# Kernel tuning notes

Hardware: AMD Instinct MI355X
Metric: run time of the kernel (lower is better)

## Reference

```python
import jax, jax.numpy as jnp
import numpy as np

INSTANCES = 4
ALPHA = 0.99
N, D_IN, C = 4096, 512, 512


def setup_inputs() -> dict:
    key = jax.random.key(0)
    k1, k2 = jax.random.split(key)
    x = jax.random.normal(k1, (N, D_IN), dtype=jnp.float32)
    Wb = jax.random.normal(k2, (D_IN, C), dtype=jnp.float32) / np.sqrt(D_IN).astype(np.float32)
    gamma = jnp.ones((2,), dtype=jnp.float32)
    return {"x": x, "Wb": Wb, "gamma": gamma}


def reference(x, Wb, gamma):
    # base model: linear feature extractor -> [N, C]
    f = x @ Wb
    n, c = f.shape
    f = f.reshape(n // INSTANCES, INSTANCES, c)
    probe = f[:, 0, :].reshape(-1, c)                 # [P, C]
    gallery = f[:, 1:INSTANCES, :].reshape(-1, c)     # [G, C]

    def embed(a, b):
        # pairwise squared distance via GEMM (no [len(a),len(b),C] tensor)
        d2 = (jnp.sum(a * a, axis=1)[:, None]
              + jnp.sum(b * b, axis=1)[None, :]
              - 2.0 * (a @ b.T)) / c
        return jnp.stack([jnp.exp(-gamma[0] * d2), gamma[1] * d2], axis=-1)

    p_g = embed(probe, gallery)     # [P, G, 2]
    g_g = embed(gallery, gallery)   # [G, G, 2]
    G = g_g.shape[0]

    gg0 = g_g[:, :, 0]
    # D = diag(1 / off-diagonal row sums); A = D @ gg0
    off_rowsum = jnp.sum(gg0, axis=1) - jnp.diagonal(gg0)
    A = gg0 / off_rowsum[:, None]
    # closed-form random-walk fixed point: (1-alpha) * (I - alpha A)^-1, then transpose
    A = (1.0 - ALPHA) * jnp.linalg.inv(jnp.eye(G, dtype=gg0.dtype) - ALPHA * A)
    A = A.T

    pg0 = p_g[:, :, 0] @ A          # rescored probe-gallery scores
    p_g = p_g.at[:, :, 0].set(pg0)

    score = jnp.concatenate([p_g.reshape(-1, 2), g_g.reshape(-1, 2)], axis=0)
    return score
```

## Files before the change

### kernel.cpp

```cpp
#include <hip/hip_runtime.h>

typedef unsigned short u16;
typedef short short8v __attribute__((ext_vector_type(8)));
typedef float f32x4 __attribute__((ext_vector_type(4)));
typedef float f32x2 __attribute__((ext_vector_type(2)));
typedef unsigned short u16x4 __attribute__((ext_vector_type(4)));

#define ALPHA_C 0.99f
#define NITER 2
#define WS_NEEDED 67500000UL

__device__ __forceinline__ u16 f2bf(float f){
  union { float f; unsigned u; } v; v.f = f;
  unsigned r = (v.u + 0x7FFFu + ((v.u >> 16) & 1u)) >> 16;
  return (u16)r;
}
__device__ __forceinline__ float bf2f(u16 u){
  union { unsigned u; float f; } v; v.u = ((unsigned)u) << 16;
  return v.f;
}

__device__ __forceinline__ void gload16(const void* g, void* l){
  __builtin_amdgcn_global_load_lds(
    (const __attribute__((address_space(1))) unsigned*)g,
    (__attribute__((address_space(3))) unsigned*)l, 16, 0, 0);
}

__device__ __forceinline__ float blockSumBcast(float v){
  #pragma unroll
  for(int off=32; off>0; off>>=1) v += __shfl_down(v, off, 64);
  __shared__ float sm[4];
  __shared__ float res;
  int w = threadIdx.x >> 6;
  if((threadIdx.x & 63)==0) sm[w] = v;
  __syncthreads();
  if(threadIdx.x==0) res = sm[0]+sm[1]+sm[2]+sm[3];
  __syncthreads();
  return res;
}

__global__ void k_canary(float* out){ out[0] = 12345.0f; }

__global__ void k_wbt(const float* __restrict__ Wb, u16* __restrict__ Wbt){
  __shared__ float t[32][33];
  int bx = blockIdx.x & 15, by = blockIdx.x >> 4;
  int tx = threadIdx.x & 31, ty = threadIdx.x >> 5;
  #pragma unroll
  for(int i=0;i<32;i+=8)
    t[ty+i][tx] = Wb[(by*32+ty+i)*512 + bx*32+tx];
  __syncthreads();
  #pragma unroll
  for(int i=0;i<32;i+=8)
    Wbt[(bx*32+ty+i)*512 + by*32 + tx] = f2bf(t[tx][ty+i]);
}

__global__ void k_f2bf8(const float* __restrict__ in, u16* __restrict__ out, int n8){
  int i = blockIdx.x*256 + threadIdx.x;
  if(i >= n8) return;
  f32x4 a = *reinterpret_cast<const f32x4*>(in + (size_t)i*8);
  f32x4 b = *reinterpret_cast<const f32x4*>(in + (size_t)i*8 + 4);
  short8v o;
  o[0]=(short)f2bf(a[0]); o[1]=(short)f2bf(a[1]); o[2]=(short)f2bf(a[2]); o[3]=(short)f2bf(a[3]);
  o[4]=(short)f2bf(b[0]); o[5]=(short)f2bf(b[1]); o[6]=(short)f2bf(b[2]); o[7]=(short)f2bf(b[3]);
  *reinterpret_cast<short8v*>(out + (size_t)i*8) = o;
}

__global__ void __launch_bounds__(256) k_gemm(
    int epi,
    const u16* __restrict__ A, const u16* __restrict__ B,
    int kld, int nbn, int bps, int kspan,
    const float* __restrict__ nrmA, const float* __restrict__ nrmB,
    const float* __restrict__ gamma,
    u16* __restrict__ u0, u16* __restrict__ u1,
    float* __restrict__ fo0,
    float* __restrict__ f0, const float* __restrict__ f1)
{
  int bid = blockIdx.x;
  int slice, brow, bcol;
  if(epi==3){
    int L = (bid & 7)*96 + (bid >> 3);
    slice = L / 192;
    int l = L - slice*192;
    bcol = l >> 3;
    brow = l & 7;
  } else if(epi==4){
    int L = (bid & 7)*96 + (bid >> 3);
    slice = 0;
    if(L < 576){ epi = 1; brow = L / 24; bcol = L % 24; }
    else { epi = 2; int l = L - 576; brow = l / 24; bcol = l % 24; A = u1; nrmA = f1; }
  } else {
    slice = bid / bps; int rem = bid % bps;
    brow = rem / nbn; bcol = rem % nbn;
  }
  int t = threadIdx.x;
  int w = t >> 6, l = t & 63;
  int wr = w >> 1, wc = w & 1;
  const int l15 = l & 15, l16 = l >> 4;
  int k0 = slice * kspan;

  __shared__ __align__(16) u16 AB[2*128*64];

  const u16* src = (w < 2) ? A + (size_t)brow*128*kld
                           : B + (size_t)bcol*128*kld;
  int half = w >> 1;
  int wq   = (w & 1) * 8;

  f32x4 acc[4][4] = {};

  for(int kk = 0; kk < kspan; kk += 64){
    int kt = k0 + kk;
    #pragma unroll
    for(int q=0;q<8;q++){
      int cb  = (wq + q)*64;
      int idx = cb + l;
      int row = idx >> 3, c8 = idx & 7;
      gload16(src + (size_t)row*kld + kt + c8*8,
              &AB[half*8192 + cb*8]);
    }
    __syncthreads();
    #pragma unroll
    for(int ks=0; ks<2; ++ks){
      short8v af[4], bfr[4];
      int ko = ks*32 + l16*8;
      #pragma unroll
      for(int i=0;i<4;i++){
        af[i]  = *reinterpret_cast<const short8v*>(&AB[(wr*64+i*16+l15)*64 + ko]);
        bfr[i] = *reinterpret_cast<const short8v*>(&AB[8192 + (wc*64+i*16+l15)*64 + ko]);
      }
      #pragma unroll
      for(int i=0;i<4;i++)
        #pragma unroll
        for(int j=0;j<4;j++)
          acc[i][j] = __builtin_amdgcn_mfma_f32_16x16x32_bf16(af[i], bfr[j], acc[i][j], 0,0,0);
    }
    __syncthreads();
  }

  float g0 = 0.f, g1 = 0.f;
  if(epi==1 || epi==2){ g0 = gamma[0]; g1 = gamma[1]; }

  #pragma unroll
  for(int i=0;i<4;i++)
  #pragma unroll
  for(int j=0;j<4;j++)
  #pragma unroll
  for(int r=0;r<4;r++){
    int m = brow*128 + wr*64 + i*16 + l16*4 + r;
    int n = bcol*128 + wc*64 + j*16 + l15;
    float c = acc[i][j][r];
    if(epi==0){
      if((m & 3) == 0) u0[(size_t)(m>>2)*512 + n] = f2bf(c);
      else             u1[(size_t)((m>>2)*3 + (m&3) - 1)*512 + n] = f2bf(c);
    } else if(epi==1){
      float d2 = (nrmA[m] + nrmB[n] - 2.f*c) * (1.f/512.f);
      float e  = __expf(-g0*d2);
      u0[(size_t)m*3072 + n] = f2bf(e);
    } else if(epi==2){
      float d2 = (nrmA[m] + nrmB[n] - 2.f*c) * (1.f/512.f);
      fo0[(size_t)m*3072 + n] = g1*d2;
    } else {
      u0[(size_t)slice*1024*3072 + (size_t)m*3072 + n] = f2bf(c);
    }
  }
}

__global__ void k_norms(const u16* __restrict__ probe, const u16* __restrict__ gal,
                        float* __restrict__ np_, float* __restrict__ ng){
  int row = blockIdx.x, t = threadIdx.x;
  const u16* src = (row < 1024) ? probe + (size_t)row*512
                                : gal + (size_t)(row-1024)*512;
  float s = 0.f;
  if(t < 64){
    short8v v = *reinterpret_cast<const short8v*>(src + t*8);
    #pragma unroll
    for(int k=0;k<8;k++){ float f = bf2f((u16)v[k]); s += f*f; }
  }
  float r = blockSumBcast(s);
  if(t==0){ if(row < 1024) np_[row] = r; else ng[row-1024] = r; }
}

__global__ void k_rowsum(const u16* __restrict__ Kb, float* __restrict__ rs,
                         float* __restrict__ sq){
  int i = blockIdx.x, t = threadIdx.x;
  const u16* row = Kb + (size_t)i*3072;
  float s = 0.f;
  for(int j = t; j < 384; j += 256){
    short8v v = *reinterpret_cast<const short8v*>(row + j*8);
    #pragma unroll
    for(int k=0;k<8;k++) s += bf2f((u16)v[k]);
  }
  float r = blockSumBcast(s);
  if(t==0){
    float d = r - bf2f(row[i]);
    rs[i] = rsqrtf(d); sq[i] = sqrtf(d);
  }
}

__global__ void k_rzinit(const float* __restrict__ D2P, const float* __restrict__ sq,
                         float* __restrict__ R, u16* __restrict__ Pdb,
                         float* __restrict__ rz, const float* __restrict__ gamma){
  int p = blockIdx.x, t = threadIdx.x;
  float c1 = -gamma[0] / gamma[1];
  size_t base = (size_t)p*3072;
  float s = 0.f;
  #pragma unroll
  for(int j=0;j<6;j++){
    int g = 2*(t + j*256);
    f32x2 dv = *reinterpret_cast<const f32x2*>(&D2P[base+g]);
    float e0 = __expf(c1*dv[0]), e1 = __expf(c1*dv[1]);
    f32x2 rv; rv[0] = sq[g]*e0; rv[1] = sq[g+1]*e1;
    *reinterpret_cast<f32x2*>(&R[base+g]) = rv;
    unsigned pk = (unsigned)f2bf(e0) | ((unsigned)f2bf(e1) << 16);
    *reinterpret_cast<unsigned*>(&Pdb[base+g]) = pk;
    s += rv[0]*rv[0] + rv[1]*rv[1];
  }
  float tot = blockSumBcast(s);
  if(t==0) rz[p] = tot;
}

__global__ void __launch_bounds__(256) k_cgstep(
    const u16* __restrict__ SPb, u16* __restrict__ Pdb,
    float* __restrict__ R, float* __restrict__ X,
    float* __restrict__ rz,
    const float* __restrict__ rs, const float* __restrict__ sq,
    const float* __restrict__ D2P, float* __restrict__ outpg,
    int first, int last)
{
  const size_t SOFF = (size_t)1024*3072;
  int p = blockIdx.x, t = threadIdx.x;
  size_t base = (size_t)p*3072;
  float pd[12], ap[12];
  float papp = 0.f;
  #pragma unroll
  for(int j=0;j<6;j++){
    int g = 2*(t + j*256);
    unsigned pu = *reinterpret_cast<const unsigned*>(&Pdb[base+g]);
    unsigned s0 = *reinterpret_cast<const unsigned*>(&SPb[base+g]);
    unsigned s1 = *reinterpret_cast<const unsigned*>(&SPb[SOFF+base+g]);
    unsigned s2 = *reinterpret_cast<const unsigned*>(&SPb[2*SOFF+base+g]);
    unsigned s3 = *reinterpret_cast<const unsigned*>(&SPb[3*SOFF+base+g]);
    float pd0 = sq[g]   * bf2f((u16)(pu & 0xffffu));
    float pd1 = sq[g+1] * bf2f((u16)(pu >> 16));
    float sv0 = (bf2f((u16)(s0&0xffffu)) + bf2f((u16)(s1&0xffffu)))
              + (bf2f((u16)(s2&0xffffu)) + bf2f((u16)(s3&0xffffu)));
    float sv1 = (bf2f((u16)(s0>>16)) + bf2f((u16)(s1>>16)))
              + (bf2f((u16)(s2>>16)) + bf2f((u16)(s3>>16)));
    pd[2*j] = pd0; pd[2*j+1] = pd1;
    ap[2*j]   = pd0 - ALPHA_C*(rs[g]  *sv0);
    ap[2*j+1] = pd1 - ALPHA_C*(rs[g+1]*sv1);
    papp += pd0*ap[2*j] + pd1*ap[2*j+1];
  }
  float pap = blockSumBcast(papp);
  float rzv = rz[p];
  float a = rzv / fmaxf(pap, 1e-30f);

  if(!last){
    float rn[12];
    float rz2p = 0.f;
    #pragma unroll
    for(int j=0;j<6;j++){
      int g = 2*(t + j*256);
      f32x2 rv2 = *reinterpret_cast<const f32x2*>(&R[base+g]);
      float rv0 = rv2[0] - a*ap[2*j];
      float rv1 = rv2[1] - a*ap[2*j+1];
      rn[2*j]=rv0; rn[2*j+1]=rv1; rz2p += rv0*rv0 + rv1*rv1;
      f32x2 xo;
      if(first){ xo[0] = a*pd[2*j]; xo[1] = a*pd[2*j+1]; }
      else{
        f32x2 xv = *reinterpret_cast<const f32x2*>(&X[base+g]);
        xo[0] = xv[0] + a*pd[2*j]; xo[1] = xv[1] + a*pd[2*j+1];
      }
      *reinterpret_cast<f32x2*>(&X[base+g]) = xo;
      f32x2 rw; rw[0]=rv0; rw[1]=rv1;
      *reinterpret_cast<f32x2*>(&R[base+g]) = rw;
    }
    float rz2 = blockSumBcast(rz2p);
    float beta = rz2 / fmaxf(rzv, 1e-30f);
    #pragma unroll
    for(int j=0;j<6;j++){
      int g = 2*(t + j*256);
      float p0 = rn[2*j]   + beta*pd[2*j];
      float p1 = rn[2*j+1] + beta*pd[2*j+1];
      unsigned pk = (unsigned)f2bf(rs[g]*p0) | ((unsigned)f2bf(rs[g+1]*p1) << 16);
      *reinterpret_cast<unsigned*>(&Pdb[base+g]) = pk;
    }
    if(t==0) rz[p] = rz2;
  } else {
    #pragma unroll
    for(int j=0;j<6;j++){
      int g = 2*(t + j*256);
      f32x2 xv = *reinterpret_cast<const f32x2*>(&X[base+g]);
      f32x2 dv = *reinterpret_cast<const f32x2*>(&D2P[base+g]);
      f32x4 o;
      o[0] = (1.0f - ALPHA_C) * (xv[0] + a*pd[2*j])   * rs[g];
      o[1] = dv[0];
      o[2] = (1.0f - ALPHA_C) * (xv[1] + a*pd[2*j+1]) * rs[g+1];
      o[3] = dv[1];
      __builtin_nontemporal_store(o, reinterpret_cast<f32x4*>(outpg + (base+g)*2));
    }
  }
}

__global__ void k_ggout(const u16* __restrict__ Kb, float* __restrict__ gg,
                        const float* __restrict__ gamma, int n4){
  int i = blockIdx.x*256 + threadIdx.x;
  if(i >= n4) return;
  float g0 = gamma[0], g1 = gamma[1];
  float ginv = -g1 / g0;
  u16x4 kv = *reinterpret_cast<const u16x4*>(Kb + (size_t)i*4);
  float e0 = bf2f(kv[0]), e1 = bf2f(kv[1]), e2 = bf2f(kv[2]), e3 = bf2f(kv[3]);
  f32x4 a, b;
  a[0] = e0; a[1] = ginv*__logf(e0);
  a[2] = e1; a[3] = ginv*__logf(e1);
  b[0] = e2; b[1] = ginv*__logf(e2);
  b[2] = e3; b[3] = ginv*__logf(e3);
  __builtin_nontemporal_store(a, reinterpret_cast<f32x4*>(gg + (size_t)i*8));
  __builtin_nontemporal_store(b, reinterpret_cast<f32x4*>(gg + (size_t)i*8 + 4));
}

extern "C" void kernel_launch(void* const* d_in, const int* in_sizes, int n_in,
                              void* d_out, int out_size, void* d_ws, size_t ws_size,
                              hipStream_t stream){
  const float* x     = (const float*)d_in[0];
  const float* Wb    = (const float*)d_in[1];
  const float* gamma = (const float*)d_in[2];
  (void)in_sizes; (void)n_in; (void)out_size;

  float* out    = (float*)d_out;
  float* out_pg = out;
  float* out_gg = out + (size_t)1024*3072*2;
  u16*   SPb    = (u16*)out_gg;

  if(ws_size < WS_NEEDED){
    k_canary<<<1, 1, 0, stream>>>(out);
    return;
  }

  char* ws = (char*)d_ws;
  size_t off = 0;
  auto alloc = [&](size_t bytes)->char*{
    char* p = ws + off; off = (off + bytes + 255) & ~(size_t)255; return p;
  };
  char*  regionA = alloc((size_t)1024*3072*4);
  u16*   xbf   = (u16*)regionA;
  u16*   wbt   = (u16*)(regionA + (size_t)4096*512*2);
  float* R     = (float*)regionA;
  u16*   probe = (u16*)  alloc((size_t)1024*512*2);
  u16*   gal   = (u16*)  alloc((size_t)3072*512*2);
  u16*   Kb    = (u16*)  alloc((size_t)3072*3072*2);
  float* np_   = (float*)alloc(1024*4);
  float* ng    = (float*)alloc(3072*4);
  float* rs    = (float*)alloc(3072*4);
  float* sq    = (float*)alloc(3072*4);
  float* rz    = (float*)alloc(1024*4);
  float* X     = (float*)alloc((size_t)1024*3072*4);
  float* D2P   = (float*)alloc((size_t)1024*3072*4);
  u16*   Pdb   = (u16*)  alloc((size_t)1024*3072*2);

  k_wbt  <<<256, 256, 0, stream>>>(Wb, wbt);
  k_f2bf8<<<1024, 256, 0, stream>>>(x, xbf, 4096*512/8);

  k_gemm<<<128, 256, 0, stream>>>(0, xbf, wbt, 512, 4, 128, 512,
      nullptr, nullptr, nullptr, probe, gal, nullptr, nullptr, nullptr);

  k_norms<<<4096, 256, 0, stream>>>(probe, gal, np_, ng);

  k_gemm<<<768, 256, 0, stream>>>(4, gal, gal, 512, 24, 768, 512,
      ng, ng, gamma, Kb, probe, D2P, nullptr, np_);

  k_rowsum<<<3072, 256, 0, stream>>>(Kb, rs, sq);

  k_rzinit<<<1024, 256, 0, stream>>>(D2P, sq, R, Pdb, rz, gamma);

  for(int it = 0; it < NITER; ++it){
    k_gemm<<<768, 256, 0, stream>>>(3, Pdb, Kb, 3072, 24, 192, 768,
        nullptr, nullptr, nullptr, SPb, nullptr, nullptr, nullptr, nullptr);
    k_cgstep<<<1024, 256, 0, stream>>>(SPb, Pdb, R, X, rz, rs, sq,
        D2P, out_pg, it==0 ? 1 : 0, it==NITER-1 ? 1 : 0);
  }

  k_ggout<<<9216, 256, 0, stream>>>(Kb, out_gg, gamma, 3072*3072/4);
}
```

Before: 249.0 us.

## Fuse norm and rowsum reductions into GEMM epilogues, store CG vectors in bf16

The k_norms and k_rowsum reduction kernels are removed. Squared row norms and off-diagonal kernel row sums are now accumulated in the GEMM epilogues with wave shuffles and atomicAdd into a zeroed buffer, and a tiny k_rowfin kernel takes the sqrt and rsqrt. The CG residual R and iterate X move from fp32 to bf16, which halves their memory traffic and shrinks the workspace. The costs are atomic contention, non-deterministic summation order, and extra rounding error in the CG state. The zeroing of the accumulator buffer is folded into k_wbt.

Measured after the change: 245.9 us. Within noise of the previous version (-1.2%).

```diff
diff --git a/kernel.cpp b/kernel.cpp
--- a/kernel.cpp
+++ b/kernel.cpp
@@ -8,7 +8,7 @@
 
 #define ALPHA_C 0.99f
 #define NITER 2
-#define WS_NEEDED 67500000UL
+#define WS_NEEDED 61000000UL
 
 __device__ __forceinline__ u16 f2bf(float f){
   union { float f; unsigned u; } v; v.f = f;
@@ -41,7 +41,10 @@
 
 __global__ void k_canary(float* out){ out[0] = 12345.0f; }
 
-__global__ void k_wbt(const float* __restrict__ Wb, u16* __restrict__ Wbt){
+__global__ void k_wbt(const float* __restrict__ Wb, u16* __restrict__ Wbt,
+                      float* __restrict__ zbuf){
+  int zi = blockIdx.x*256 + threadIdx.x;
+  if(zi < 7168) zbuf[zi] = 0.f;
   __shared__ float t[32][33];
   int bx = blockIdx.x & 15, by = blockIdx.x >> 4;
   int tx = threadIdx.x & 31, ty = threadIdx.x >> 5;
@@ -73,7 +76,8 @@
     const float* __restrict__ gamma,
     u16* __restrict__ u0, u16* __restrict__ u1,
     float* __restrict__ fo0,
-    float* __restrict__ f0, const float* __restrict__ f1)
+    float* __restrict__ fa0, float* __restrict__ fa1,
+    const float* __restrict__ f1)
 {
   int bid = blockIdx.x;
   int slice, brow, bcol;
@@ -139,6 +143,8 @@
   float g0 = 0.f, g1 = 0.f;
   if(epi==1 || epi==2){ g0 = gamma[0]; g1 = gamma[1]; }
 
+  float nacc[4][4] = {};
+
   #pragma unroll
   for(int i=0;i<4;i++)
   #pragma unroll
@@ -149,12 +155,16 @@
     int n = bcol*128 + wc*64 + j*16 + l15;
     float c = acc[i][j][r];
     if(epi==0){
-      if((m & 3) == 0) u0[(size_t)(m>>2)*512 + n] = f2bf(c);
-      else             u1[(size_t)((m>>2)*3 + (m&3) - 1)*512 + n] = f2bf(c);
+      u16 b = f2bf(c);
+      if((m & 3) == 0) u0[(size_t)(m>>2)*512 + n] = b;
+      else             u1[(size_t)((m>>2)*3 + (m&3) - 1)*512 + n] = b;
+      float v = bf2f(b);
+      nacc[i][r] += v*v;
     } else if(epi==1){
       float d2 = (nrmA[m] + nrmB[n] - 2.f*c) * (1.f/512.f);
       float e  = __expf(-g0*d2);
       u0[(size_t)m*3072 + n] = f2bf(e);
+      if(m != n) nacc[i][r] += e;
     } else if(epi==2){
       float d2 = (nrmA[m] + nrmB[n] - 2.f*c) * (1.f/512.f);
       fo0[(size_t)m*3072 + n] = g1*d2;
@@ -162,42 +172,38 @@
       u0[(size_t)slice*1024*3072 + (size_t)m*3072 + n] = f2bf(c);
     }
   }
-}
-
-__global__ void k_norms(const u16* __restrict__ probe, const u16* __restrict__ gal,
-                        float* __restrict__ np_, float* __restrict__ ng){
-  int row = blockIdx.x, t = threadIdx.x;
-  const u16* src = (row < 1024) ? probe + (size_t)row*512
-                                : gal + (size_t)(row-1024)*512;
-  float s = 0.f;
-  if(t < 64){
-    short8v v = *reinterpret_cast<const short8v*>(src + t*8);
-    #pragma unroll
-    for(int k=0;k<8;k++){ float f = bf2f((u16)v[k]); s += f*f; }
-  }
-  float r = blockSumBcast(s);
-  if(t==0){ if(row < 1024) np_[row] = r; else ng[row-1024] = r; }
-}
-
-__global__ void k_rowsum(const u16* __restrict__ Kb, float* __restrict__ rs,
+
+  if(epi <= 1){
+    #pragma unroll
+    for(int i=0;i<4;i++)
+    #pragma unroll
+    for(int r=0;r<4;r++){
+      float s = nacc[i][r];
+      #pragma unroll
+      for(int mk=1; mk<16; mk<<=1) s += __shfl_xor(s, mk, 64);
+      if(l15 == 0){
+        int m = brow*128 + wr*64 + i*16 + l16*4 + r;
+        if(epi==0){
+          if((m & 3) == 0) atomicAdd(&fa0[m>>2], s);
+          else             atomicAdd(&fa1[(m>>2)*3 + (m&3) - 1], s);
+        } else {
+          atomicAdd(&fa0[m], s);
+        }
+      }
+    }
+  }
+}
+
+__global__ void k_rowfin(const float* __restrict__ rsum, float* __restrict__ rs,
                          float* __restrict__ sq){
-  int i = blockIdx.x, t = threadIdx.x;
-  const u16* row = Kb + (size_t)i*3072;
-  float s = 0.f;
-  for(int j = t; j < 384; j += 256){
-    short8v v = *reinterpret_cast<const short8v*>(row + j*8);
-    #pragma unroll
-    for(int k=0;k<8;k++) s += bf2f((u16)v[k]);
-  }
-  float r = blockSumBcast(s);
-  if(t==0){
-    float d = r - bf2f(row[i]);
-    rs[i] = rsqrtf(d); sq[i] = sqrtf(d);
-  }
+  int i = blockIdx.x*256 + threadIdx.x;
+  if(i >= 3072) return;
+  float d = rsum[i];
+  rs[i] = rsqrtf(d); sq[i] = sqrtf(d);
 }
 
 __global__ void k_rzinit(const float* __restrict__ D2P, const float* __restrict__ sq,
-                         float* __restrict__ R, u16* __restrict__ Pdb,
+                         u16* __restrict__ Rb, u16* __restrict__ Pdb,
                          float* __restrict__ rz, const float* __restrict__ gamma){
   int p = blockIdx.x, t = threadIdx.x;
   float c1 = -gamma[0] / gamma[1];
@@ -208,11 +214,12 @@
     int g = 2*(t + j*256);
     f32x2 dv = *reinterpret_cast<const f32x2*>(&D2P[base+g]);
     float e0 = __expf(c1*dv[0]), e1 = __expf(c1*dv[1]);
-    f32x2 rv; rv[0] = sq[g]*e0; rv[1] = sq[g+1]*e1;
-    *reinterpret_cast<f32x2*>(&R[base+g]) = rv;
-    unsigned pk = (unsigned)f2bf(e0) | ((unsigned)f2bf(e1) << 16);
-    *reinterpret_cast<unsigned*>(&Pdb[base+g]) = pk;
-    s += rv[0]*rv[0] + rv[1]*rv[1];
+    float r0 = sq[g]*e0, r1 = sq[g+1]*e1;
+    *reinterpret_cast<unsigned*>(&Rb[base+g]) =
+        (unsigned)f2bf(r0) | ((unsigned)f2bf(r1) << 16);
+    *reinterpret_cast<unsigned*>(&Pdb[base+g]) =
+        (unsigned)f2bf(e0) | ((unsigned)f2bf(e1) << 16);
+    s += r0*r0 + r1*r1;
   }
   float tot = blockSumBcast(s);
   if(t==0) rz[p] = tot;
@@ -220,7 +227,7 @@
 
 __global__ void __launch_bounds__(256) k_cgstep(
     const u16* __restrict__ SPb, u16* __restrict__ Pdb,
-    float* __restrict__ R, float* __restrict__ X,
+    u16* __restrict__ Rb, u16* __restrict__ Xb,
     float* __restrict__ rz,
     const float* __restrict__ rs, const float* __restrict__ sq,
     const float* __restrict__ D2P, float* __restrict__ outpg,
@@ -260,19 +267,21 @@
     #pragma unroll
     for(int j=0;j<6;j++){
       int g = 2*(t + j*256);
-      f32x2 rv2 = *reinterpret_cast<const f32x2*>(&R[base+g]);
-      float rv0 = rv2[0] - a*ap[2*j];
-      float rv1 = rv2[1] - a*ap[2*j+1];
+      unsigned ru = *reinterpret_cast<const unsigned*>(&Rb[base+g]);
+      float rv0 = bf2f((u16)(ru & 0xffffu)) - a*ap[2*j];
+      float rv1 = bf2f((u16)(ru >> 16))     - a*ap[2*j+1];
       rn[2*j]=rv0; rn[2*j+1]=rv1; rz2p += rv0*rv0 + rv1*rv1;
-      f32x2 xo;
-      if(first){ xo[0] = a*pd[2*j]; xo[1] = a*pd[2*j+1]; }
+      float xv0, xv1;
+      if(first){ xv0 = a*pd[2*j]; xv1 = a*pd[2*j+1]; }
       else{
-        f32x2 xv = *reinterpret_cast<const f32x2*>(&X[base+g]);
-        xo[0] = xv[0] + a*pd[2*j]; xo[1] = xv[1] + a*pd[2*j+1];
+        unsigned xu = *reinterpret_cast<const unsigned*>(&Xb[base+g]);
+        xv0 = bf2f((u16)(xu & 0xffffu)) + a*pd[2*j];
+        xv1 = bf2f((u16)(xu >> 16))     + a*pd[2*j+1];
       }
-      *reinterpret_cast<f32x2*>(&X[base+g]) = xo;
-      f32x2 rw; rw[0]=rv0; rw[1]=rv1;
-      *reinterpret_cast<f32x2*>(&R[base+g]) = rw;
+      *reinterpret_cast<unsigned*>(&Xb[base+g]) =
+          (unsigned)f2bf(xv0) | ((unsigned)f2bf(xv1) << 16);
+      *reinterpret_cast<unsigned*>(&Rb[base+g]) =
+          (unsigned)f2bf(rv0) | ((unsigned)f2bf(rv1) << 16);
     }
     float rz2 = blockSumBcast(rz2p);
     float beta = rz2 / fmaxf(rzv, 1e-30f);
@@ -289,12 +298,12 @@
     #pragma unroll
     for(int j=0;j<6;j++){
       int g = 2*(t + j*256);
-      f32x2 xv = *reinterpret_cast<const f32x2*>(&X[base+g]);
+      unsigned xu = *reinterpret_cast<const unsigned*>(&Xb[base+g]);
       f32x2 dv = *reinterpret_cast<const f32x2*>(&D2P[base+g]);
       f32x4 o;
-      o[0] = (1.0f - ALPHA_C) * (xv[0] + a*pd[2*j])   * rs[g];
+      o[0] = (1.0f - ALPHA_C) * (bf2f((u16)(xu & 0xffffu)) + a*pd[2*j])   * rs[g];
       o[1] = dv[0];
-      o[2] = (1.0f - ALPHA_C) * (xv[1] + a*pd[2*j+1]) * rs[g+1];
+      o[2] = (1.0f - ALPHA_C) * (bf2f((u16)(xu >> 16))     + a*pd[2*j+1]) * rs[g+1];
       o[3] = dv[1];
       __builtin_nontemporal_store(o, reinterpret_cast<f32x4*>(outpg + (base+g)*2));
     }
@@ -341,41 +350,40 @@
   auto alloc = [&](size_t bytes)->char*{
     char* p = ws + off; off = (off + bytes + 255) & ~(size_t)255; return p;
   };
-  char*  regionA = alloc((size_t)1024*3072*4);
+  char*  regionA = alloc((size_t)4096*512*2 + (size_t)512*512*2 + 512);
   u16*   xbf   = (u16*)regionA;
   u16*   wbt   = (u16*)(regionA + (size_t)4096*512*2);
-  float* R     = (float*)regionA;
+  u16*   Rb    = (u16*)regionA;
   u16*   probe = (u16*)  alloc((size_t)1024*512*2);
   u16*   gal   = (u16*)  alloc((size_t)3072*512*2);
   u16*   Kb    = (u16*)  alloc((size_t)3072*3072*2);
   float* np_   = (float*)alloc(1024*4);
   float* ng    = (float*)alloc(3072*4);
+  float* rsum  = (float*)alloc(3072*4);
   float* rs    = (float*)alloc(3072*4);
   float* sq    = (float*)alloc(3072*4);
   float* rz    = (float*)alloc(1024*4);
-  float* X     = (float*)alloc((size_t)1024*3072*4);
+  u16*   Xb    = (u16*)  alloc((size_t)1024*3072*2);
   float* D2P   = (float*)alloc((size_t)1024*3072*4);
   u16*   Pdb   = (u16*)  alloc((size_t)1024*3072*2);
 
-  k_wbt  <<<256, 256, 0, stream>>>(Wb, wbt);
+  k_wbt  <<<256, 256, 0, stream>>>(Wb, wbt, np_);
   k_f2bf8<<<1024, 256, 0, stream>>>(x, xbf, 4096*512/8);
 
   k_gemm<<<128, 256, 0, stream>>>(0, xbf, wbt, 512, 4, 128, 512,
-      nullptr, nullptr, nullptr, probe, gal, nullptr, nullptr, nullptr);
-
-  k_norms<<<4096, 256, 0, stream>>>(probe, gal, np_, ng);
+      nullptr, nullptr, nullptr, probe, gal, nullptr, np_, ng, nullptr);
 
   k_gemm<<<768, 256, 0, stream>>>(4, gal, gal, 512, 24, 768, 512,
-      ng, ng, gamma, Kb, probe, D2P, nullptr, np_);
-
-  k_rowsum<<<3072, 256, 0, stream>>>(Kb, rs, sq);
-
-  k_rzinit<<<1024, 256, 0, stream>>>(D2P, sq, R, Pdb, rz, gamma);
+      ng, ng, gamma, Kb, probe, D2P, rsum, nullptr, np_);
+
+  k_rowfin<<<12, 256, 0, stream>>>(rsum, rs, sq);
+
+  k_rzinit<<<1024, 256, 0, stream>>>(D2P, sq, Rb, Pdb, rz, gamma);
 
   for(int it = 0; it < NITER; ++it){
     k_gemm<<<768, 256, 0, stream>>>(3, Pdb, Kb, 3072, 24, 192, 768,
-        nullptr, nullptr, nullptr, SPb, nullptr, nullptr, nullptr, nullptr);
-    k_cgstep<<<1024, 256, 0, stream>>>(SPb, Pdb, R, X, rz, rs, sq,
+        nullptr, nullptr, nullptr, SPb, nullptr, nullptr, nullptr, nullptr, nullptr);
+    k_cgstep<<<1024, 256, 0, stream>>>(SPb, Pdb, Rb, Xb, rz, rs, sq,
         D2P, out_pg, it==0 ? 1 : 0, it==NITER-1 ? 1 : 0);
   }
 
```
